# Performance work log

Hardware: AMD Instinct MI355X
Metric: run time of the kernel (lower is better)

The kernel has to match this reference:

```python
import jax, jax.numpy as jnp
import numpy as np

OBSERVE = 30

def setup_inputs() -> dict:
    key = jax.random.key(0)
    k1, k2, k3, k4 = jax.random.split(key, 4)
    B, T = 8192, 2048
    u = jax.random.normal(k1, (B, T, 1), dtype=jnp.float32)
    x0 = jax.random.normal(k2, (B, OBSERVE), dtype=jnp.float32)
    # scale weights small so the linear AR recurrence stays stable over T steps
    W_x = jax.random.normal(k3, (OBSERVE, 1), dtype=jnp.float32) * 0.05
    W_f = jax.random.normal(k4, (1, 1), dtype=jnp.float32)
    return {"u": u, "x0": x0, "W_x": W_x, "W_f": W_f}


def reference(u, x0, W_x, W_f):
    # u: [B, T, 1]; x0: [B, observe] initial shift-register state.
    # Per step (matching the Keras cell):
    #   out = x_set @ W_x + u_t @ W_f            -> [B, 1]
    #   x_set <- concat(x_set[:, 1:], out)        (shift register)
    def step(x_set, u_t):
        out = x_set @ W_x + u_t @ W_f            # [B, 1]
        x_new = jnp.concatenate([x_set[:, 1:], out], axis=1)
        return x_new, out

    u_tbf = jnp.swapaxes(u, 0, 1)                # [T, B, 1]
    _, outs = jax.lax.scan(step, x0, u_tbf)      # outs: [T, B, 1]
    return jnp.swapaxes(outs, 0, 1)              # [B, T, 1]
```

## Files before the change

kernel.cpp:

```cpp
#include <hip/hip_runtime.h>

#define NB   8192
#define NT   2048
#define OBS  30
#define CCH  32
#define RPB  8
#define NTHR 256
#define CSTR 68

__device__ __forceinline__ float step6(float (&r)[32], const float (&wx)[OBS],
                                       int j, float uwf) {
  float a0 = fmaf(wx[0], r[(j + 0) & 31], uwf);
  float a1 = wx[1] * r[(j + 1) & 31];
  float a2 = wx[2] * r[(j + 2) & 31];
  float a3 = wx[3] * r[(j + 3) & 31];
  float a4 = wx[4] * r[(j + 4) & 31];
  float a5 = wx[5] * r[(j + 5) & 31];
  #pragma unroll
  for (int i = 6; i < OBS; i += 6) {
    a0 = fmaf(wx[i],     r[(j + i)     & 31], a0);
    a1 = fmaf(wx[i + 1], r[(j + i + 1) & 31], a1);
    a2 = fmaf(wx[i + 2], r[(j + i + 2) & 31], a2);
    a3 = fmaf(wx[i + 3], r[(j + i + 3) & 31], a3);
    a4 = fmaf(wx[i + 4], r[(j + i + 4) & 31], a4);
    a5 = fmaf(wx[i + 5], r[(j + i + 5) & 31], a5);
  }
  float out = ((a0 + a1) + (a2 + a3)) + (a4 + a5);
  r[(j + 30) & 31] = out;
  return out;
}

__global__ void __launch_bounds__(NTHR, 2)
k_fused(const float* __restrict__ u, const float* __restrict__ x0,
        const float* __restrict__ Wx, const float* __restrict__ Wf,
        float* __restrict__ out) {
  __shared__ float tile[RPB * CCH * CSTR];
  __shared__ float Cb[64 * 33];
  __shared__ float sbuf[RPB * 32];
  const int tid  = threadIdx.x;
  const int wv   = tid >> 6;
  const int lane = tid & 63;
  const int half = lane >> 5;
  const int k    = lane & 31;
  const int row0 = blockIdx.x * RPB;
  const int lr   = wv * 2 + half;
  const int row  = row0 + lr;

  float wx[OBS];
  #pragma unroll
  for (int i = 0; i < OBS; ++i) wx[i] = Wx[i];
  const float wf = Wf[0];

  float4 stg[16];
  const float* ub = u + (size_t)row0 * NT;
  #pragma unroll
  for (int i = 0; i < 16; ++i) {
    int v = i * NTHR + tid, rr = v >> 9, p = v & 511;
    stg[i] = *(const float4*)(ub + (size_t)rr * NT + 4 * p);
  }

  {
    float r[32];
    #pragma unroll
    for (int i = 0; i < 32; ++i) r[i] = (k < OBS && i == k) ? 1.f : 0.f;
    #pragma unroll
    for (int q = 0; q < 16; ++q)
      #pragma unroll
      for (int e = 0; e < 4; ++e) {
        float o = step6(r, wx, (4 * q + e) & 31, 0.f);
        if (tid < OBS) Cb[(4 * q + e) * 33 + tid] = o;
      }
  }
  if (k < OBS) sbuf[lr * 32 + k] = x0[(size_t)row * OBS + k];

  #pragma unroll
  for (int i = 0; i < 16; ++i) {
    int v = i * NTHR + tid, rr = v >> 9, p = v & 511;
    int c = p >> 4, q = p & 15;
    *(float4*)(&tile[(rr * CCH + c) * CSTR + 4 * q]) = stg[i];
  }
  __syncthreads();

  {
    float r[32];
    #pragma unroll
    for (int i = 0; i < 32; ++i) r[i] = 0.f;
    float* tc = &tile[tid * CSTR];
    #pragma unroll
    for (int q = 0; q < 16; ++q) {
      float4 u4 = *(const float4*)(tc + 4 * q);
      float4 o4;
      o4.x = step6(r, wx, (4 * q + 0) & 31, wf * u4.x);
      o4.y = step6(r, wx, (4 * q + 1) & 31, wf * u4.y);
      o4.z = step6(r, wx, (4 * q + 2) & 31, wf * u4.z);
      o4.w = step6(r, wx, (4 * q + 3) & 31, wf * u4.w);
      *(float4*)(tc + 4 * q) = o4;
    }
  }
  __syncthreads();

  float c0[OBS], c1[OBS];
  #pragma unroll
  for (int i = 0; i < OBS; ++i) c0[i] = Cb[(2 * k) * 33 + i];
  #pragma unroll
  for (int i = 0; i < OBS; ++i) c1[i] = Cb[(2 * k + 1) * 33 + i];

  float* sl = &sbuf[lr * 32];
  const float* trow = &tile[(lr * CCH) * CSTR];
  float* orow = out + (size_t)row * NT;
  #pragma unroll 1
  for (int c = 0; c < CCH; ++c) {
    float sv[32];
    #pragma unroll
    for (int q = 0; q < 8; ++q) {
      float4 v = *(const float4*)(sl + 4 * q);
      sv[4 * q] = v.x; sv[4 * q + 1] = v.y;
      sv[4 * q + 2] = v.z; sv[4 * q + 3] = v.w;
    }
    float2 pq = *(const float2*)(&trow[c * CSTR + 2 * k]);
    float a0 = fmaf(c0[0], sv[0], pq.x);
    float a1 = c0[1] * sv[1];
    float a2 = c0[2] * sv[2];
    float b0 = fmaf(c1[0], sv[0], pq.y);
    float b1 = c1[1] * sv[1];
    float b2 = c1[2] * sv[2];
    #pragma unroll
    for (int i = 3; i < OBS; i += 3) {
      a0 = fmaf(c0[i],     sv[i],     a0);
      a1 = fmaf(c0[i + 1], sv[i + 1], a1);
      a2 = fmaf(c0[i + 2], sv[i + 2], a2);
      b0 = fmaf(c1[i],     sv[i],     b0);
      b1 = fmaf(c1[i + 1], sv[i + 1], b1);
      b2 = fmaf(c1[i + 2], sv[i + 2], b2);
    }
    float t0 = a0 + (a1 + a2);
    float t1 = b0 + (b1 + b2);
    if (k >= 17)
      *(float2*)(&sl[2 * k - 34]) = make_float2(t0, t1);
    *(float2*)(&orow[c * 64 + 2 * k]) = make_float2(t0, t1);
    __builtin_amdgcn_wave_barrier();
  }
}

extern "C" void kernel_launch(void* const* d_in, const int* in_sizes, int n_in,
                              void* d_out, int out_size, void* d_ws, size_t ws_size,
                              hipStream_t stream) {
  const float* u  = (const float*)d_in[0];
  const float* x0 = (const float*)d_in[1];
  const float* Wx = (const float*)d_in[2];
  const float* Wf = (const float*)d_in[3];
  float* out = (float*)d_out;

  hipLaunchKernelGGL(k_fused, dim3(NB / RPB), dim3(NTHR), 0, stream,
                     u, x0, Wx, Wf, out);
}
```

Baseline: 51.64 us.

## Double chunk length to 128 and cut sequential carry steps in half

Chunk length grows from 64 to 128 steps, so each row needs only 16 serial carry-propagation iterations instead of 32. Each 32-lane group now handles one row with four outputs per lane, reusing the tile buffer for the impulse-response table. In exchange, only half the threads run the local-chunk scan (each doing twice the steps), each lane holds four coefficient vectors in registers, and a single wave computes the longer 128-step response table.

```diff
diff --git a/kernel.cpp b/kernel.cpp
--- a/kernel.cpp
+++ b/kernel.cpp
@@ -3,10 +3,11 @@
 #define NB   8192
 #define NT   2048
 #define OBS  30
-#define CCH  32
+#define LCH  128
+#define CCH  16
 #define RPB  8
 #define NTHR 256
-#define CSTR 68
+#define CSTR 132
 
 __device__ __forceinline__ float step6(float (&r)[32], const float (&wx)[OBS],
                                        int j, float uwf) {
@@ -30,26 +31,37 @@
   return out;
 }
 
+__device__ __forceinline__ float dot30(const float (&c)[OBS],
+                                       const float (&sv)[32], float p) {
+  float a0 = fmaf(c[0], sv[0], p);
+  float a1 = c[1] * sv[1];
+  float a2 = c[2] * sv[2];
+  #pragma unroll
+  for (int i = 3; i < OBS; i += 3) {
+    a0 = fmaf(c[i],     sv[i],     a0);
+    a1 = fmaf(c[i + 1], sv[i + 1], a1);
+    a2 = fmaf(c[i + 2], sv[i + 2], a2);
+  }
+  return a0 + (a1 + a2);
+}
+
 __global__ void __launch_bounds__(NTHR, 2)
 k_fused(const float* __restrict__ u, const float* __restrict__ x0,
         const float* __restrict__ Wx, const float* __restrict__ Wf,
         float* __restrict__ out) {
   __shared__ float tile[RPB * CCH * CSTR];
-  __shared__ float Cb[64 * 33];
   __shared__ float sbuf[RPB * 32];
   const int tid  = threadIdx.x;
   const int wv   = tid >> 6;
-  const int lane = tid & 63;
-  const int half = lane >> 5;
-  const int k    = lane & 31;
+  const int g    = tid >> 5;
+  const int k    = tid & 31;
   const int row0 = blockIdx.x * RPB;
-  const int lr   = wv * 2 + half;
-  const int row  = row0 + lr;
 
   float wx[OBS];
   #pragma unroll
   for (int i = 0; i < OBS; ++i) wx[i] = Wx[i];
   const float wf = Wf[0];
+  float x0v = (k < OBS) ? x0[(size_t)(row0 + g) * OBS + k] : 0.f;
 
   float4 stg[16];
   const float* ub = u + (size_t)row0 * NT;
@@ -59,35 +71,47 @@
     stg[i] = *(const float4*)(ub + (size_t)rr * NT + 4 * p);
   }
 
-  {
+  if (wv == 0) {
     float r[32];
     #pragma unroll
-    for (int i = 0; i < 32; ++i) r[i] = (k < OBS && i == k) ? 1.f : 0.f;
+    for (int i = 0; i < 32; ++i) r[i] = (tid < OBS && i == tid) ? 1.f : 0.f;
     #pragma unroll
-    for (int q = 0; q < 16; ++q)
+    for (int q = 0; q < 32; ++q)
       #pragma unroll
       for (int e = 0; e < 4; ++e) {
         float o = step6(r, wx, (4 * q + e) & 31, 0.f);
-        if (tid < OBS) Cb[(4 * q + e) * 33 + tid] = o;
+        if (tid < OBS) tile[(4 * q + e) * 33 + tid] = o;
       }
   }
-  if (k < OBS) sbuf[lr * 32 + k] = x0[(size_t)row * OBS + k];
+  __syncthreads();
+
+  float c0[OBS], c1[OBS], c2[OBS], c3[OBS];
+  #pragma unroll
+  for (int i = 0; i < OBS; ++i) c0[i] = tile[(4 * k + 0) * 33 + i];
+  #pragma unroll
+  for (int i = 0; i < OBS; ++i) c1[i] = tile[(4 * k + 1) * 33 + i];
+  #pragma unroll
+  for (int i = 0; i < OBS; ++i) c2[i] = tile[(4 * k + 2) * 33 + i];
+  #pragma unroll
+  for (int i = 0; i < OBS; ++i) c3[i] = tile[(4 * k + 3) * 33 + i];
+  sbuf[g * 32 + k] = x0v;
+  __syncthreads();
 
   #pragma unroll
   for (int i = 0; i < 16; ++i) {
     int v = i * NTHR + tid, rr = v >> 9, p = v & 511;
-    int c = p >> 4, q = p & 15;
+    int c = p >> 5, q = p & 31;
     *(float4*)(&tile[(rr * CCH + c) * CSTR + 4 * q]) = stg[i];
   }
   __syncthreads();
 
-  {
+  if (tid < RPB * CCH) {
     float r[32];
     #pragma unroll
     for (int i = 0; i < 32; ++i) r[i] = 0.f;
     float* tc = &tile[tid * CSTR];
     #pragma unroll
-    for (int q = 0; q < 16; ++q) {
+    for (int q = 0; q < 32; ++q) {
       float4 u4 = *(const float4*)(tc + 4 * q);
       float4 o4;
       o4.x = step6(r, wx, (4 * q + 0) & 31, wf * u4.x);
@@ -99,15 +123,9 @@
   }
   __syncthreads();
 
-  float c0[OBS], c1[OBS];
-  #pragma unroll
-  for (int i = 0; i < OBS; ++i) c0[i] = Cb[(2 * k) * 33 + i];
-  #pragma unroll
-  for (int i = 0; i < OBS; ++i) c1[i] = Cb[(2 * k + 1) * 33 + i];
-
-  float* sl = &sbuf[lr * 32];
-  const float* trow = &tile[(lr * CCH) * CSTR];
-  float* orow = out + (size_t)row * NT;
+  float* sl = &sbuf[g * 32];
+  const float* trow = &tile[(g * CCH) * CSTR];
+  float* orow = out + (size_t)(row0 + g) * NT;
   #pragma unroll 1
   for (int c = 0; c < CCH; ++c) {
     float sv[32];
@@ -117,27 +135,14 @@
       sv[4 * q] = v.x; sv[4 * q + 1] = v.y;
       sv[4 * q + 2] = v.z; sv[4 * q + 3] = v.w;
     }
-    float2 pq = *(const float2*)(&trow[c * CSTR + 2 * k]);
-    float a0 = fmaf(c0[0], sv[0], pq.x);
-    float a1 = c0[1] * sv[1];
-    float a2 = c0[2] * sv[2];
-    float b0 = fmaf(c1[0], sv[0], pq.y);
-    float b1 = c1[1] * sv[1];
-    float b2 = c1[2] * sv[2];
-    #pragma unroll
-    for (int i = 3; i < OBS; i += 3) {
-      a0 = fmaf(c0[i],     sv[i],     a0);
-      a1 = fmaf(c0[i + 1], sv[i + 1], a1);
-      a2 = fmaf(c0[i + 2], sv[i + 2], a2);
-      b0 = fmaf(c1[i],     sv[i],     b0);
-      b1 = fmaf(c1[i + 1], sv[i + 1], b1);
-      b2 = fmaf(c1[i + 2], sv[i + 2], b2);
-    }
-    float t0 = a0 + (a1 + a2);
-    float t1 = b0 + (b1 + b2);
-    if (k >= 17)
-      *(float2*)(&sl[2 * k - 34]) = make_float2(t0, t1);
-    *(float2*)(&orow[c * 64 + 2 * k]) = make_float2(t0, t1);
+    float4 p4 = *(const float4*)(&trow[c * CSTR + 4 * k]);
+    float o0 = dot30(c0, sv, p4.x);
+    float o1 = dot30(c1, sv, p4.y);
+    float o2 = dot30(c2, sv, p4.z);
+    float o3 = dot30(c3, sv, p4.w);
+    if (k >= 25) *(float2*)(&sl[4 * k - 98]) = make_float2(o0, o1);
+    if (k >= 24) *(float2*)(&sl[4 * k - 96]) = make_float2(o2, o3);
+    *(float4*)(&orow[c * LCH + 4 * k]) = make_float4(o0, o1, o2, o3);
     __builtin_amdgcn_wave_barrier();
   }
 }
```

Result: slower. 87.39 us (+69.2%).
